# Kernel tuning notes

Hardware: AMD Instinct MI355X
Metric: run time of the kernel (lower is better)

Reference implementation:

```python
import jax, jax.numpy as jnp
import numpy as np

B, T, I, H, O = 512, 1024, 80, 160, 1


def setup_inputs() -> dict:
    key = jax.random.key(0)
    ks = jax.random.split(key, 11)
    s = 1.0 / np.sqrt(H)  # pytorch default init scale
    return {
        "x": jax.random.normal(ks[0], (B, T, I), dtype=jnp.float32),
        "W_ih0": jax.random.normal(ks[1], (4 * H, I), dtype=jnp.float32) * s,
        "W_hh0": jax.random.normal(ks[2], (4 * H, H), dtype=jnp.float32) * s,
        "b_ih0": jax.random.normal(ks[3], (4 * H,), dtype=jnp.float32) * s,
        "b_hh0": jax.random.normal(ks[4], (4 * H,), dtype=jnp.float32) * s,
        "W_ih1": jax.random.normal(ks[5], (4 * H, H), dtype=jnp.float32) * s,
        "W_hh1": jax.random.normal(ks[6], (4 * H, H), dtype=jnp.float32) * s,
        "b_ih1": jax.random.normal(ks[7], (4 * H,), dtype=jnp.float32) * s,
        "b_hh1": jax.random.normal(ks[8], (4 * H,), dtype=jnp.float32) * s,
        "W_out": jax.random.normal(ks[9], (O, H), dtype=jnp.float32) * s,
        "b_out": jax.random.normal(ks[10], (O,), dtype=jnp.float32) * s,
    }


def _lstm_cell(xt, h, c, W_ih, W_hh, b_ih, b_hh):
    # gates: [B, 4H], pytorch order i, f, g, o
    gates = xt @ W_ih.T + b_ih + h @ W_hh.T + b_hh
    i, f, g, o = jnp.split(gates, 4, axis=-1)
    c_new = jax.nn.sigmoid(f) * c + jax.nn.sigmoid(i) * jnp.tanh(g)
    h_new = jax.nn.sigmoid(o) * jnp.tanh(c_new)
    return h_new, c_new


def reference(x, W_ih0, W_hh0, b_ih0, b_hh0, W_ih1, W_hh1, b_ih1, b_hh1, W_out, b_out):
    Bx = x.shape[0]
    h0 = jnp.zeros((Bx, H), x.dtype)
    init = (h0, h0, h0, h0)  # (h_l0, c_l0, h_l1, c_l1)

    def step(carry, xt):
        h0_, c0_, h1_, c1_ = carry
        h0n, c0n = _lstm_cell(xt, h0_, c0_, W_ih0, W_hh0, b_ih0, b_hh0)
        h1n, c1n = _lstm_cell(h0n, h1_, c1_, W_ih1, W_hh1, b_ih1, b_hh1)
        y = jax.nn.relu(h1n @ W_out.T + b_out)  # [B, O]
        return (h0n, c0n, h1n, c1n), y

    xs = jnp.swapaxes(x, 0, 1)  # [T, B, I]
    _, ys = jax.lax.scan(step, init, xs)  # [T, B, O]
    return jnp.swapaxes(ys, 0, 1)  # [B, T, O]
```

## Files before the change

### kernel.cpp

```cpp
#include <hip/hip_runtime.h>
#include <stdint.h>


#define TT 1024
#define BATCH 512
#define II 80
#define HH 160

constexpr int BB    = 16;
constexpr int NGRP  = BATCH / BB;
constexpr int NW    = 8;
constexpr int NTHR  = NW * 64;
constexpr int NTILE = 5;
constexpr int DEPTH = 32;
constexpr int HP    = 168;
constexpr int XP    = 88;

typedef __attribute__((ext_vector_type(8))) short s8b;
typedef __attribute__((ext_vector_type(4))) short s4b;
typedef __attribute__((ext_vector_type(4))) float f4;

constexpr int SLOT_U64 = 960;
constexpr size_t OFF_RING = 4096;
constexpr size_t RING_STRIDE = (size_t)DEPTH * SLOT_U64 * 8;
constexpr size_t WS_ZERO = OFF_RING + (size_t)NGRP * RING_STRIDE;

constexpr int HSH_OFF = 81920;
constexpr int H0L_OFF = 92672;
constexpr int YP_OFF  = 103424;
constexpr int BS_OFF  = 104448;
constexpr int SMEM_SZ = 107648;

constexpr float KLOG2E  = 1.4426950408889634f;
constexpr float KLOG2E2 = 2.8853900817779268f;

__device__ __forceinline__ short f2bf(float x){
  uint32_t u = __builtin_bit_cast(uint32_t, x);
  u = (u + 0x7FFFu + ((u >> 16) & 1u)) >> 16;
  return (short)u;
}
__device__ __forceinline__ float rcpf(float x){ return __builtin_amdgcn_rcpf(x); }
__device__ __forceinline__ float exp2f_(float x){ return __builtin_amdgcn_exp2f(x); }
__device__ __forceinline__ float sig2(float a){ return rcpf(1.f + exp2f_(-a)); }
__device__ __forceinline__ float tanh2(float a){ return 1.f - 2.f*rcpf(exp2f_(a) + 1.f); }

__device__ __forceinline__ f4 mfma16(s8b a, s8b b, f4 c){
  return __builtin_amdgcn_mfma_f32_16x16x32_bf16(a, b, c, 0, 0, 0);
}

__device__ __forceinline__ s8b pack8(float4 a, float4 b){
  s8b r;
  r[0]=f2bf(a.x); r[1]=f2bf(a.y); r[2]=f2bf(a.z); r[3]=f2bf(a.w);
  r[4]=f2bf(b.x); r[5]=f2bf(b.y); r[6]=f2bf(b.z); r[7]=f2bf(b.w);
  return r;
}
__device__ __forceinline__ float4 ld4(const float* p){ return *(const float4*)p; }
__device__ __forceinline__ s8b wfrag_s(const float* p, float sc){
  float4 a = ld4(p), b = ld4(p+4);
  s8b r;
  r[0]=f2bf(a.x*sc); r[1]=f2bf(a.y*sc); r[2]=f2bf(a.z*sc); r[3]=f2bf(a.w*sc);
  r[4]=f2bf(b.x*sc); r[5]=f2bf(b.y*sc); r[6]=f2bf(b.z*sc); r[7]=f2bf(b.w*sc);
  return r;
}

__device__ __forceinline__ void st64(unsigned long long* p, unsigned long long v){
  __hip_atomic_store(p, v, __ATOMIC_RELAXED, __HIP_MEMORY_SCOPE_AGENT);
}
__device__ __forceinline__ unsigned long long ld64(const unsigned long long* p){
  return __hip_atomic_load(p, __ATOMIC_RELAXED, __HIP_MEMORY_SCOPE_AGENT);
}
__device__ __forceinline__ void poll_ge(int* p, int& shadow, int target, int lane){
  while (shadow < target){
    int v = 0;
    if (lane == 0) v = __hip_atomic_load(p, __ATOMIC_ACQUIRE, __HIP_MEMORY_SCOPE_AGENT);
    shadow = __shfl(v, 0, 64);
    if (shadow < target) __builtin_amdgcn_s_sleep(2);
  }
}

__global__ __launch_bounds__(NTHR, 1)
void lstm2(const float* __restrict__ x,
           const float* __restrict__ Wih0, const float* __restrict__ Whh0,
           const float* __restrict__ bih0, const float* __restrict__ bhh0,
           const float* __restrict__ Wih1, const float* __restrict__ Whh1,
           const float* __restrict__ bih1, const float* __restrict__ bhh1,
           const float* __restrict__ Wout, const float* __restrict__ bout,
           float* __restrict__ out, char* __restrict__ ws)
{
  extern __shared__ char smem[];
  const int tid = threadIdx.x;
  const int w   = tid >> 6;
  const int l   = tid & 63;
  const int lq  = l >> 4;
  const int lr  = l & 15;
  const int q   = l & 3;
  const int h2  = (l >> 2) & 3;
  const int stage = blockIdx.x >> 5;
  const int gid   = blockIdx.x & 31;
  const int b0    = gid * BB;
  const int li    = w*64 + l;
  const float wsc = (q == 2) ? KLOG2E2 : KLOG2E;

  int* prog = (int*)ws + gid;
  unsigned long long* ring =
      (unsigned long long*)(ws + OFF_RING + (size_t)gid * RING_STRIDE);

  short* hsh = (short*)(smem + HSH_OFF);
  const s8b zf = {};

  if (stage == 0){
    short* xsh = (short*)(smem + H0L_OFF);
    s8b Wh[NTILE][5], Wi2[NTILE];
    f4 biasv[NTILE];
    #pragma unroll
    for (int s = 0; s < NTILE; ++s){
      const int ct = w + 8*s;
      const int wrow = q*HH + 4*ct + h2;
      const int u = 4*ct + lq;
      #pragma unroll
      for (int g = 0; g < 4; ++g)
        biasv[s][g] = (bih0[g*HH + u] + bhh0[g*HH + u]) * (g == 2 ? KLOG2E2 : KLOG2E);
      #pragma unroll
      for (int kt = 0; kt < 2; ++kt)
        *(s8b*)(smem + ((w*10 + s*2 + kt) << 10) + (l << 4)) =
            wfrag_s(Wih0 + (size_t)wrow*II + kt*32 + lq*8, wsc);
      Wi2[s] = (lq < 2) ? wfrag_s(Wih0 + (size_t)wrow*II + 64 + lq*8, wsc) : zf;
      #pragma unroll
      for (int kt = 0; kt < 5; ++kt)
        Wh[s][kt] = wfrag_s(Whh0 + (size_t)wrow*HH + kt*32 + lq*8, wsc);
    }
    if (w == 7){
      const float* xp = x + (size_t)(b0 + lr) * TT * II + (l>>4)*20;
      short* xd = xsh + lr*XP + (l>>4)*20;
      #pragma unroll
      for (int i = 0; i < 5; ++i){
        float4 a = ld4(xp + i*4);
        s4b p; p[0]=f2bf(a.x); p[1]=f2bf(a.y); p[2]=f2bf(a.z); p[3]=f2bf(a.w);
        *(s4b*)(xd + i*4) = p;
      }
    }
    __syncthreads();

    s8b h0a[5];
    #pragma unroll
    for (int kt = 0; kt < 5; ++kt) h0a[kt] = zf;
    float c0[NTILE] = {0.f,0.f,0.f,0.f,0.f};

    s8b xa[3];
    {
      const short* xr = xsh + lr*XP;
      xa[0] = *(const s8b*)&xr[lq*8];
      xa[1] = *(const s8b*)&xr[32 + lq*8];
      xa[2] = (lq < 2) ? *(const s8b*)&xr[64 + lq*8] : zf;
    }
    f4 accx[NTILE];
    #pragma unroll
    for (int s = 0; s < NTILE; ++s){
      accx[s] = biasv[s];
      accx[s] = mfma16(*(const s8b*)(smem + ((w*10 + s*2 + 0) << 10) + (l << 4)), xa[0], accx[s]);
      accx[s] = mfma16(*(const s8b*)(smem + ((w*10 + s*2 + 1) << 10) + (l << 4)), xa[1], accx[s]);
      accx[s] = mfma16(Wi2[s], xa[2], accx[s]);
    }

    int credB = 0;
    for (int t = 0; t < TT; ++t){
      float4 xl0, xl1, xl2, xl3, xl4;
      if (w == 7 && t+1 < TT){
        const float* xp = x + (size_t)(b0 + lr) * TT * II + (size_t)(t+1)*II + (l>>4)*20;
        xl0 = ld4(xp); xl1 = ld4(xp+4); xl2 = ld4(xp+8); xl3 = ld4(xp+12); xl4 = ld4(xp+16);
      }

      if (t >= DEPTH && credB < t - DEPTH + 1)
        poll_ge(prog, credB, t - DEPTH + 1, l);

      short* hb = hsh + (t&1)*16*HP;
      #pragma unroll
      for (int kt = 0; kt < 5; ++kt)
        #pragma unroll
        for (int s = 0; s < NTILE; ++s)
          accx[s] = mfma16(Wh[s][kt], h0a[kt], accx[s]);
      #pragma unroll
      for (int s = 0; s < NTILE; ++s){
        const float i_ = sig2(accx[s][0]);
        const float f_ = sig2(accx[s][1]);
        const float g_ = tanh2(accx[s][2]);
        const float o_ = sig2(accx[s][3]);
        const float cn = f_*c0[s] + i_*g_;
        c0[s] = cn;
        const float h = o_*(1.f - 2.f*rcpf(exp2f_(KLOG2E2*cn) + 1.f));
        hb[lr*HP + 4*(w + 8*s) + lq] = f2bf(h);
      }
      if (w == 7 && t+1 < TT){
        short* xd = xsh + ((t+1)&1)*16*XP + lr*XP + (l>>4)*20;
        float4 a[5] = {xl0, xl1, xl2, xl3, xl4};
        #pragma unroll
        for (int i = 0; i < 5; ++i){
          s4b p; p[0]=f2bf(a[i].x); p[1]=f2bf(a[i].y); p[2]=f2bf(a[i].z); p[3]=f2bf(a[i].w);
          *(s4b*)(xd + i*4) = p;
        }
      }
      __syncthreads();
      #pragma unroll
      for (int kt = 0; kt < 5; ++kt)
        h0a[kt] = *(const s8b*)&hb[lr*HP + kt*32 + lq*8];
      if (w < 5){
        const s8b hf = h0a[w];
        const unsigned long long tg = (unsigned long long)(t+1);
        unsigned long long u0 = (unsigned long long)(unsigned short)hf[0]
                              | ((unsigned long long)(unsigned short)hf[1] << 16)
                              | ((unsigned long long)(unsigned short)hf[2] << 32)
                              | (tg << 48);
        unsigned long long u1 = (unsigned long long)(unsigned short)hf[3]
                              | ((unsigned long long)(unsigned short)hf[4] << 16)
                              | ((unsigned long long)(unsigned short)hf[5] << 32)
                              | (tg << 48);
        unsigned long long u2 = (unsigned long long)(unsigned short)hf[6]
                              | ((unsigned long long)(unsigned short)hf[7] << 16)
                              | (tg << 32) | (tg << 48);
        unsigned long long* sl = ring + (size_t)(t & (DEPTH-1))*SLOT_U64;
        st64(sl + li, u0); st64(sl + 320 + li, u1); st64(sl + 640 + li, u2);
      }
      {
        const short* xr = xsh + ((t+1)&1)*16*XP + lr*XP;
        xa[0] = *(const s8b*)&xr[lq*8];
        xa[1] = *(const s8b*)&xr[32 + lq*8];
        xa[2] = (lq < 2) ? *(const s8b*)&xr[64 + lq*8] : zf;
      }
      #pragma unroll
      for (int s = 0; s < NTILE; ++s){
        accx[s] = biasv[s];
        accx[s] = mfma16(*(const s8b*)(smem + ((w*10 + s*2 + 0) << 10) + (l << 4)), xa[0], accx[s]);
        accx[s] = mfma16(*(const s8b*)(smem + ((w*10 + s*2 + 1) << 10) + (l << 4)), xa[1], accx[s]);
        accx[s] = mfma16(Wi2[s], xa[2], accx[s]);
      }
    }
  }
  else {
    short* h0l = (short*)(smem + H0L_OFF);
    float* ypart = (float*)(smem + YP_OFF);
    f4* bias4 = (f4*)(smem + BS_OFF);
    for (int i = tid; i < HH; i += NTHR){
      f4 b;
      #pragma unroll
      for (int g = 0; g < 4; ++g)
        b[g] = (bih1[g*HH + i] + bhh1[g*HH + i]) * (g == 2 ? KLOG2E2 : KLOG2E);
      bias4[i] = b;
    }
    s8b Wi[NTILE][3], Wh[NTILE][5];
    float woutv[NTILE];
    #pragma unroll
    for (int s = 0; s < NTILE; ++s){
      const int ct = w + 8*s;
      const int wrow = q*HH + 4*ct + h2;
      woutv[s] = Wout[4*ct + lq];
      #pragma unroll
      for (int kt = 0; kt < 5; ++kt)
        Wh[s][kt] = wfrag_s(Whh1 + (size_t)wrow*HH + kt*32 + lq*8, wsc);
      #pragma unroll
      for (int kt = 0; kt < 3; ++kt)
        Wi[s][kt] = wfrag_s(Wih1 + (size_t)wrow*HH + kt*32 + lq*8, wsc);
      #pragma unroll
      for (int kt = 3; kt < 5; ++kt)
        *(s8b*)(smem + ((w*10 + s*2 + (kt-3)) << 10) + (l << 4)) =
            wfrag_s(Wih1 + (size_t)wrow*HH + kt*32 + lq*8, wsc);
    }
    const float bo = bout[0];
    s8b h1a[5];
    #pragma unroll
    for (int kt = 0; kt < 5; ++kt) h1a[kt] = zf;
    float c1[NTILE] = {0.f,0.f,0.f,0.f,0.f};

    unsigned long long in0 = 0, in1 = 0, in2 = 0;
    if (w < 5){
      const unsigned long long* src = ring;
      in0 = ld64(src + li); in1 = ld64(src + 320 + li); in2 = ld64(src + 640 + li);
      bool ok = ((int)(in0>>48)==1) && ((int)(in1>>48)==1) && ((int)(in2>>48)==1);
      while (__ballot(ok) != ~0ull){
        __builtin_amdgcn_s_sleep(1);
        in0 = ld64(src + li); in1 = ld64(src + 320 + li); in2 = ld64(src + 640 + li);
        ok = ((int)(in0>>48)==1) && ((int)(in1>>48)==1) && ((int)(in2>>48)==1);
      }
      s8b v;
      v[0]=(short)in0; v[1]=(short)(in0>>16); v[2]=(short)(in0>>32);
      v[3]=(short)in1; v[4]=(short)(in1>>16); v[5]=(short)(in1>>32);
      v[6]=(short)in2; v[7]=(short)(in2>>16);
      *(s8b*)&h0l[lr*HP + w*32 + lq*8] = v;
      const unsigned long long* p1 = ring + SLOT_U64;
      in0 = ld64(p1 + li); in1 = ld64(p1 + 320 + li); in2 = ld64(p1 + 640 + li);
    }
    __syncthreads();

    f4 accx[NTILE];
    {
      const short* hp = h0l;
      #pragma unroll
      for (int s = 0; s < NTILE; ++s)
        accx[s] = bias4[4*(w + 8*s) + lq];
      #pragma unroll
      for (int kt = 0; kt < 3; ++kt){
        const s8b hf = *(const s8b*)&hp[lr*HP + kt*32 + lq*8];
        #pragma unroll
        for (int s = 0; s < NTILE; ++s) accx[s] = mfma16(Wi[s][kt], hf, accx[s]);
      }
      #pragma unroll
      for (int kt = 3; kt < 5; ++kt){
        const s8b hf = *(const s8b*)&hp[lr*HP + kt*32 + lq*8];
        #pragma unroll
        for (int s = 0; s < NTILE; ++s)
          accx[s] = mfma16(*(const s8b*)(smem + ((w*10 + s*2 + (kt-3)) << 10) + (l << 4)), hf, accx[s]);
      }
    }

    for (int t = 0; t < TT; ++t){
      short* hb = hsh + (t&1)*16*HP;
      #pragma unroll
      for (int kt = 0; kt < 5; ++kt)
        #pragma unroll
        for (int s = 0; s < NTILE; ++s)
          accx[s] = mfma16(Wh[s][kt], h1a[kt], accx[s]);

      if (w < 5 && t+1 < TT){
        const int tg = t+2;
        const unsigned long long* src = ring + (size_t)((t+1) & (DEPTH-1))*SLOT_U64;
        bool ok = ((int)(in0>>48)==tg) && ((int)(in1>>48)==tg) && ((int)(in2>>48)==tg);
        while (__ballot(ok) != ~0ull){
          __builtin_amdgcn_s_sleep(1);
          in0 = ld64(src + li); in1 = ld64(src + 320 + li); in2 = ld64(src + 640 + li);
          ok = ((int)(in0>>48)==tg) && ((int)(in1>>48)==tg) && ((int)(in2>>48)==tg);
        }
        s8b v;
        v[0]=(short)in0; v[1]=(short)(in0>>16); v[2]=(short)(in0>>32);
        v[3]=(short)in1; v[4]=(short)(in1>>16); v[5]=(short)(in1>>32);
        v[6]=(short)in2; v[7]=(short)(in2>>16);
        *(s8b*)&h0l[((t+1)&1)*16*HP + lr*HP + w*32 + lq*8] = v;
      }

      float ysum = 0.f;
      #pragma unroll
      for (int s = 0; s < NTILE; ++s){
        const float i_ = sig2(accx[s][0]);
        const float f_ = sig2(accx[s][1]);
        const float g_ = tanh2(accx[s][2]);
        const float o_ = sig2(accx[s][3]);
        const float cn = f_*c1[s] + i_*g_;
        c1[s] = cn;
        const float h = o_*(1.f - 2.f*rcpf(exp2f_(KLOG2E2*cn) + 1.f));
        hb[lr*HP + 4*(w + 8*s) + lq] = f2bf(h);
        ysum += h * woutv[s];
      }
      ysum += __shfl_xor(ysum, 16, 64);
      ysum += __shfl_xor(ysum, 32, 64);
      if (l < 16) ypart[(t&1)*128 + w*16 + l] = ysum;

      __syncthreads();
      #pragma unroll
      for (int kt = 0; kt < 5; ++kt)
        h1a[kt] = *(const s8b*)&hb[lr*HP + kt*32 + lq*8];
      if (w == 0 && l < 16){
        float s_ = bo;
        #pragma unroll
        for (int ww = 0; ww < NW; ++ww) s_ += ypart[(t&1)*128 + ww*16 + l];
        out[(size_t)(b0 + l)*TT + t] = fmaxf(s_, 0.f);
      }
      {
        const short* hp = h0l + ((t+1)&1)*16*HP;
        #pragma unroll
        for (int s = 0; s < NTILE; ++s)
          accx[s] = bias4[4*(w + 8*s) + lq];
        #pragma unroll
        for (int kt = 0; kt < 3; ++kt){
          const s8b hf = *(const s8b*)&hp[lr*HP + kt*32 + lq*8];
          #pragma unroll
          for (int s = 0; s < NTILE; ++s) accx[s] = mfma16(Wi[s][kt], hf, accx[s]);
        }
        #pragma unroll
        for (int kt = 3; kt < 5; ++kt){
          const s8b hf = *(const s8b*)&hp[lr*HP + kt*32 + lq*8];
          #pragma unroll
          for (int s = 0; s < NTILE; ++s)
            accx[s] = mfma16(*(const s8b*)(smem + ((w*10 + s*2 + (kt-3)) << 10) + (l << 4)), hf, accx[s]);
        }
      }
      if (w < 5 && t+2 < TT){
        const unsigned long long* p =
            ring + (size_t)((t+2) & (DEPTH-1))*SLOT_U64;
        in0 = ld64(p + li); in1 = ld64(p + 320 + li); in2 = ld64(p + 640 + li);
      }
      if (((t & 7) == 7) && tid == 0)
        __hip_atomic_store(prog, t+1, __ATOMIC_RELEASE, __HIP_MEMORY_SCOPE_AGENT);
    }
  }
}

extern "C" void kernel_launch(void* const* d_in, const int* in_sizes, int n_in,
                              void* d_out, int out_size, void* d_ws, size_t ws_size,
                              hipStream_t stream)
{
  (void)in_sizes; (void)n_in; (void)out_size; (void)ws_size;
  (void)hipFuncSetAttribute(reinterpret_cast<const void*>(lstm2),
                            hipFuncAttributeMaxDynamicSharedMemorySize, SMEM_SZ);
  (void)hipMemsetAsync(d_ws, 0, WS_ZERO, stream);
  lstm2<<<dim3(NGRP*2), dim3(NTHR), SMEM_SZ, stream>>>(
      (const float*)d_in[0],
      (const float*)d_in[1], (const float*)d_in[2],
      (const float*)d_in[3], (const float*)d_in[4],
      (const float*)d_in[5], (const float*)d_in[6],
      (const float*)d_in[7], (const float*)d_in[8],
      (const float*)d_in[9], (const float*)d_in[10],
      (float*)d_out, (char*)d_ws);
}
```

Baseline: 4.659 ms.

## Pack two batch groups per 1024-thread block sharing LDS weight fragments

Each block now runs two 16-sample batch groups, one per 512-thread half. The grid shrinks from 64 to 32 blocks, and the LDS-resident weight fragments are written once and shared by both halves. The aim is to use fewer CUs and overlap two independent recurrences on each CU to hide latency. In exchange, each SIMD carries twice the waves, which cuts the per-thread register budget and risks spills of the large register-held weight arrays. __syncthreads now also couples the two independent halves, so one half's stall holds up the other.

```diff
diff --git a/kernel.cpp b/kernel.cpp
--- a/kernel.cpp
+++ b/kernel.cpp
@@ -10,7 +10,7 @@
 constexpr int BB    = 16;
 constexpr int NGRP  = BATCH / BB;
 constexpr int NW    = 8;
-constexpr int NTHR  = NW * 64;
+constexpr int NTHR  = 1024;
 constexpr int NTILE = 5;
 constexpr int DEPTH = 32;
 constexpr int HP    = 168;
@@ -25,11 +25,7 @@
 constexpr size_t RING_STRIDE = (size_t)DEPTH * SLOT_U64 * 8;
 constexpr size_t WS_ZERO = OFF_RING + (size_t)NGRP * RING_STRIDE;
 
-constexpr int HSH_OFF = 81920;
-constexpr int H0L_OFF = 92672;
-constexpr int YP_OFF  = 103424;
-constexpr int BS_OFF  = 104448;
-constexpr int SMEM_SZ = 107648;
+constexpr int SMEM_SZ = 131072;
 
 constexpr float KLOG2E  = 1.4426950408889634f;
 constexpr float KLOG2E2 = 2.8853900817779268f;
@@ -48,12 +44,6 @@
   return __builtin_amdgcn_mfma_f32_16x16x32_bf16(a, b, c, 0, 0, 0);
 }
 
-__device__ __forceinline__ s8b pack8(float4 a, float4 b){
-  s8b r;
-  r[0]=f2bf(a.x); r[1]=f2bf(a.y); r[2]=f2bf(a.z); r[3]=f2bf(a.w);
-  r[4]=f2bf(b.x); r[5]=f2bf(b.y); r[6]=f2bf(b.z); r[7]=f2bf(b.w);
-  return r;
-}
 __device__ __forceinline__ float4 ld4(const float* p){ return *(const float4*)p; }
 __device__ __forceinline__ s8b wfrag_s(const float* p, float sc){
   float4 a = ld4(p), b = ld4(p+4);
@@ -88,48 +78,53 @@
            float* __restrict__ out, char* __restrict__ ws)
 {
   extern __shared__ char smem[];
-  const int tid = threadIdx.x;
-  const int w   = tid >> 6;
-  const int l   = tid & 63;
-  const int lq  = l >> 4;
-  const int lr  = l & 15;
-  const int q   = l & 3;
-  const int h2  = (l >> 2) & 3;
-  const int stage = blockIdx.x >> 5;
-  const int gid   = blockIdx.x & 31;
+  const int tid  = threadIdx.x;
+  const int w    = tid >> 6;
+  const int half = w >> 3;
+  const int w8   = w & 7;
+  const int l    = tid & 63;
+  const int lq   = l >> 4;
+  const int lr   = l & 15;
+  const int q    = l & 3;
+  const int h2   = (l >> 2) & 3;
+  const int stage = blockIdx.x >> 4;
+  const int bi    = blockIdx.x & 15;
+  const int gid   = bi*2 + half;
   const int b0    = gid * BB;
-  const int li    = w*64 + l;
+  const int li    = w8*64 + l;
   const float wsc = (q == 2) ? KLOG2E2 : KLOG2E;
 
   int* prog = (int*)ws + gid;
   unsigned long long* ring =
       (unsigned long long*)(ws + OFF_RING + (size_t)gid * RING_STRIDE);
 
-  short* hsh = (short*)(smem + HSH_OFF);
   const s8b zf = {};
 
   if (stage == 0){
-    short* xsh = (short*)(smem + H0L_OFF);
+    short* hsh = (short*)(smem + 81920 + half*10752);
+    short* xsh = (short*)(smem + 103424 + half*5632);
     s8b Wh[NTILE][5], Wi2[NTILE];
     f4 biasv[NTILE];
     #pragma unroll
     for (int s = 0; s < NTILE; ++s){
-      const int ct = w + 8*s;
+      const int ct = w8 + 8*s;
       const int wrow = q*HH + 4*ct + h2;
       const int u = 4*ct + lq;
       #pragma unroll
       for (int g = 0; g < 4; ++g)
         biasv[s][g] = (bih0[g*HH + u] + bhh0[g*HH + u]) * (g == 2 ? KLOG2E2 : KLOG2E);
-      #pragma unroll
-      for (int kt = 0; kt < 2; ++kt)
-        *(s8b*)(smem + ((w*10 + s*2 + kt) << 10) + (l << 4)) =
-            wfrag_s(Wih0 + (size_t)wrow*II + kt*32 + lq*8, wsc);
+      if (half == 0){
+        #pragma unroll
+        for (int kt = 0; kt < 2; ++kt)
+          *(s8b*)(smem + ((w8*10 + s*2 + kt) << 10) + (l << 4)) =
+              wfrag_s(Wih0 + (size_t)wrow*II + kt*32 + lq*8, wsc);
+      }
       Wi2[s] = (lq < 2) ? wfrag_s(Wih0 + (size_t)wrow*II + 64 + lq*8, wsc) : zf;
       #pragma unroll
       for (int kt = 0; kt < 5; ++kt)
         Wh[s][kt] = wfrag_s(Whh0 + (size_t)wrow*HH + kt*32 + lq*8, wsc);
     }
-    if (w == 7){
+    if (w8 == 7){
       const float* xp = x + (size_t)(b0 + lr) * TT * II + (l>>4)*20;
       short* xd = xsh + lr*XP + (l>>4)*20;
       #pragma unroll
@@ -157,15 +152,15 @@
     #pragma unroll
     for (int s = 0; s < NTILE; ++s){
       accx[s] = biasv[s];
-      accx[s] = mfma16(*(const s8b*)(smem + ((w*10 + s*2 + 0) << 10) + (l << 4)), xa[0], accx[s]);
-      accx[s] = mfma16(*(const s8b*)(smem + ((w*10 + s*2 + 1) << 10) + (l << 4)), xa[1], accx[s]);
+      accx[s] = mfma16(*(const s8b*)(smem + ((w8*10 + s*2 + 0) << 10) + (l << 4)), xa[0], accx[s]);
+      accx[s] = mfma16(*(const s8b*)(smem + ((w8*10 + s*2 + 1) << 10) + (l << 4)), xa[1], accx[s]);
       accx[s] = mfma16(Wi2[s], xa[2], accx[s]);
     }
 
     int credB = 0;
     for (int t = 0; t < TT; ++t){
       float4 xl0, xl1, xl2, xl3, xl4;
-      if (w == 7 && t+1 < TT){
+      if (w8 == 7 && t+1 < TT){
         const float* xp = x + (size_t)(b0 + lr) * TT * II + (size_t)(t+1)*II + (l>>4)*20;
         xl0 = ld4(xp); xl1 = ld4(xp+4); xl2 = ld4(xp+8); xl3 = ld4(xp+12); xl4 = ld4(xp+16);
       }
@@ -188,9 +183,9 @@
         const float cn = f_*c0[s] + i_*g_;
         c0[s] = cn;
         const float h = o_*(1.f - 2.f*rcpf(exp2f_(KLOG2E2*cn) + 1.f));
-        hb[lr*HP + 4*(w + 8*s) + lq] = f2bf(h);
-      }
-      if (w == 7 && t+1 < TT){
+        hb[lr*HP + 4*(w8 + 8*s) + lq] = f2bf(h);
+      }
+      if (w8 == 7 && t+1 < TT){
         short* xd = xsh + ((t+1)&1)*16*XP + lr*XP + (l>>4)*20;
         float4 a[5] = {xl0, xl1, xl2, xl3, xl4};
         #pragma unroll
@@ -203,8 +198,8 @@
       #pragma unroll
       for (int kt = 0; kt < 5; ++kt)
         h0a[kt] = *(const s8b*)&hb[lr*HP + kt*32 + lq*8];
-      if (w < 5){
-        const s8b hf = h0a[w];
+      if (w8 < 5){
+        const s8b hf = h0a[w8];
         const unsigned long long tg = (unsigned long long)(t+1);
         unsigned long long u0 = (unsigned long long)(unsigned short)hf[0]
                               | ((unsigned long long)(unsigned short)hf[1] << 16)
@@ -229,16 +224,17 @@
       #pragma unroll
       for (int s = 0; s < NTILE; ++s){
         accx[s] = biasv[s];
-        accx[s] = mfma16(*(const s8b*)(smem + ((w*10 + s*2 + 0) << 10) + (l << 4)), xa[0], accx[s]);
-        accx[s] = mfma16(*(const s8b*)(smem + ((w*10 + s*2 + 1) << 10) + (l << 4)), xa[1], accx[s]);
+        accx[s] = mfma16(*(const s8b*)(smem + ((w8*10 + s*2 + 0) << 10) + (l << 4)), xa[0], accx[s]);
+        accx[s] = mfma16(*(const s8b*)(smem + ((w8*10 + s*2 + 1) << 10) + (l << 4)), xa[1], accx[s]);
         accx[s] = mfma16(Wi2[s], xa[2], accx[s]);
       }
     }
   }
   else {
-    short* h0l = (short*)(smem + H0L_OFF);
-    float* ypart = (float*)(smem + YP_OFF);
-    f4* bias4 = (f4*)(smem + BS_OFF);
+    short* h0l   = (short*)(smem + 81920  + half*10752);
+    short* hsh   = (short*)(smem + 103424 + half*10752);
+    float* ypart = (float*)(smem + 124928 + half*1024);
+    f4* bias4    = (f4*)(smem + 126976);
     for (int i = tid; i < HH; i += NTHR){
       f4 b;
       #pragma unroll
@@ -250,7 +246,7 @@
     float woutv[NTILE];
     #pragma unroll
     for (int s = 0; s < NTILE; ++s){
-      const int ct = w + 8*s;
+      const int ct = w8 + 8*s;
       const int wrow = q*HH + 4*ct + h2;
       woutv[s] = Wout[4*ct + lq];
       #pragma unroll
@@ -259,10 +255,12 @@
       #pragma unroll
       for (int kt = 0; kt < 3; ++kt)
         Wi[s][kt] = wfrag_s(Wih1 + (size_t)wrow*HH + kt*32 + lq*8, wsc);
-      #pragma unroll
-      for (int kt = 3; kt < 5; ++kt)
-        *(s8b*)(smem + ((w*10 + s*2 + (kt-3)) << 10) + (l << 4)) =
-            wfrag_s(Wih1 + (size_t)wrow*HH + kt*32 + lq*8, wsc);
+      if (half == 0){
+        #pragma unroll
+        for (int kt = 3; kt < 5; ++kt)
+          *(s8b*)(smem + ((w8*10 + s*2 + (kt-3)) << 10) + (l << 4)) =
+              wfrag_s(Wih1 + (size_t)wrow*HH + kt*32 + lq*8, wsc);
+      }
     }
     const float bo = bout[0];
     s8b h1a[5];
@@ -271,7 +269,7 @@
     float c1[NTILE] = {0.f,0.f,0.f,0.f,0.f};
 
     unsigned long long in0 = 0, in1 = 0, in2 = 0;
-    if (w < 5){
+    if (w8 < 5){
       const unsigned long long* src = ring;
       in0 = ld64(src + li); in1 = ld64(src + 320 + li); in2 = ld64(src + 640 + li);
       bool ok = ((int)(in0>>48)==1) && ((int)(in1>>48)==1) && ((int)(in2>>48)==1);
@@ -284,7 +282,7 @@
       v[0]=(short)in0; v[1]=(short)(in0>>16); v[2]=(short)(in0>>32);
       v[3]=(short)in1; v[4]=(short)(in1>>16); v[5]=(short)(in1>>32);
       v[6]=(short)in2; v[7]=(short)(in2>>16);
-      *(s8b*)&h0l[lr*HP + w*32 + lq*8] = v;
+      *(s8b*)&h0l[lr*HP + w8*32 + lq*8] = v;
       const unsigned long long* p1 = ring + SLOT_U64;
       in0 = ld64(p1 + li); in1 = ld64(p1 + 320 + li); in2 = ld64(p1 + 640 + li);
     }
@@ -295,7 +293,7 @@
       const short* hp = h0l;
       #pragma unroll
       for (int s = 0; s < NTILE; ++s)
-        accx[s] = bias4[4*(w + 8*s) + lq];
+        accx[s] = bias4[4*(w8 + 8*s) + lq];
       #pragma unroll
       for (int kt = 0; kt < 3; ++kt){
         const s8b hf = *(const s8b*)&hp[lr*HP + kt*32 + lq*8];
@@ -307,7 +305,7 @@
         const s8b hf = *(const s8b*)&hp[lr*HP + kt*32 + lq*8];
         #pragma unroll
         for (int s = 0; s < NTILE; ++s)
-          accx[s] = mfma16(*(const s8b*)(smem + ((w*10 + s*2 + (kt-3)) << 10) + (l << 4)), hf, accx[s]);
+          accx[s] = mfma16(*(const s8b*)(smem + ((w8*10 + s*2 + (kt-3)) << 10) + (l << 4)), hf, accx[s]);
       }
     }
 
@@ -319,7 +317,7 @@
         for (int s = 0; s < NTILE; ++s)
           accx[s] = mfma16(Wh[s][kt], h1a[kt], accx[s]);
 
-      if (w < 5 && t+1 < TT){
+      if (w8 < 5 && t+1 < TT){
         const int tg = t+2;
         const unsigned long long* src = ring + (size_t)((t+1) & (DEPTH-1))*SLOT_U64;
         bool ok = ((int)(in0>>48)==tg) && ((int)(in1>>48)==tg) && ((int)(in2>>48)==tg);
@@ -332,7 +330,7 @@
         v[0]=(short)in0; v[1]=(short)(in0>>16); v[2]=(short)(in0>>32);
         v[3]=(short)in1; v[4]=(short)(in1>>16); v[5]=(short)(in1>>32);
         v[6]=(short)in2; v[7]=(short)(in2>>16);
-        *(s8b*)&h0l[((t+1)&1)*16*HP + lr*HP + w*32 + lq*8] = v;
+        *(s8b*)&h0l[((t+1)&1)*16*HP + lr*HP + w8*32 + lq*8] = v;
       }
 
       float ysum = 0.f;
@@ -345,18 +343,18 @@
         const float cn = f_*c1[s] + i_*g_;
         c1[s] = cn;
         const float h = o_*(1.f - 2.f*rcpf(exp2f_(KLOG2E2*cn) + 1.f));
-        hb[lr*HP + 4*(w + 8*s) + lq] = f2bf(h);
+        hb[lr*HP + 4*(w8 + 8*s) + lq] = f2bf(h);
         ysum += h * woutv[s];
       }
       ysum += __shfl_xor(ysum, 16, 64);
       ysum += __shfl_xor(ysum, 32, 64);
-      if (l < 16) ypart[(t&1)*128 + w*16 + l] = ysum;
+      if (l < 16) ypart[(t&1)*128 + w8*16 + l] = ysum;
 
       __syncthreads();
       #pragma unroll
       for (int kt = 0; kt < 5; ++kt)
         h1a[kt] = *(const s8b*)&hb[lr*HP + kt*32 + lq*8];
-      if (w == 0 && l < 16){
+      if (w8 == 0 && l < 16){
         float s_ = bo;
         #pragma unroll
         for (int ww = 0; ww < NW; ++ww) s_ += ypart[(t&1)*128 + ww*16 + l];
@@ -366,7 +364,7 @@
         const short* hp = h0l + ((t+1)&1)*16*HP;
         #pragma unroll
         for (int s = 0; s < NTILE; ++s)
-          accx[s] = bias4[4*(w + 8*s) + lq];
+          accx[s] = bias4[4*(w8 + 8*s) + lq];
         #pragma unroll
         for (int kt = 0; kt < 3; ++kt){
           const s8b hf = *(const s8b*)&hp[lr*HP + kt*32 + lq*8];
@@ -378,15 +376,15 @@
           const s8b hf = *(const s8b*)&hp[lr*HP + kt*32 + lq*8];
           #pragma unroll
           for (int s = 0; s < NTILE; ++s)
-            accx[s] = mfma16(*(const s8b*)(smem + ((w*10 + s*2 + (kt-3)) << 10) + (l << 4)), hf, accx[s]);
+            accx[s] = mfma16(*(const s8b*)(smem + ((w8*10 + s*2 + (kt-3)) << 10) + (l << 4)), hf, accx[s]);
         }
       }
-      if (w < 5 && t+2 < TT){
+      if (w8 < 5 && t+2 < TT){
         const unsigned long long* p =
             ring + (size_t)((t+2) & (DEPTH-1))*SLOT_U64;
         in0 = ld64(p + li); in1 = ld64(p + 320 + li); in2 = ld64(p + 640 + li);
       }
-      if (((t & 7) == 7) && tid == 0)
+      if (((t & 7) == 7) && w8 == 0 && l == 0)
         __hip_atomic_store(prog, t+1, __ATOMIC_RELEASE, __HIP_MEMORY_SCOPE_AGENT);
     }
   }
@@ -400,7 +398,7 @@
   (void)hipFuncSetAttribute(reinterpret_cast<const void*>(lstm2),
                             hipFuncAttributeMaxDynamicSharedMemorySize, SMEM_SZ);
   (void)hipMemsetAsync(d_ws, 0, WS_ZERO, stream);
-  lstm2<<<dim3(NGRP*2), dim3(NTHR), SMEM_SZ, stream>>>(
+  lstm2<<<dim3(NGRP), dim3(NTHR), SMEM_SZ, stream>>>(
       (const float*)d_in[0],
       (const float*)d_in[1], (const float*)d_in[2],
       (const float*)d_in[3], (const float*)d_in[4],
```

After: 18.00 ms. 286% more time.
